# Kernel optimization log

Measured on AMD Instinct MI355X. Metric: run time of the kernel, lower is better.

The kernel has to match this reference:

```python
import jax, jax.numpy as jnp
import numpy as np

SLIDING_WINDOW = 2048
NUM_SINK = 4


def make_mask(q_len, k_len, dtype=jnp.float32):
    # positions of queries in the key axis
    q_pos = jnp.arange(k_len - q_len, k_len)[:, None]  # [Q,1]
    k_pos = jnp.arange(k_len)[None, :]                 # [1,K]
    causal = k_pos <= q_pos
    in_window = k_pos >= (q_pos - SLIDING_WINDOW + 1)
    is_sink = k_pos < NUM_SINK
    allowed = causal & (in_window | is_sink)
    return jnp.where(allowed, jnp.zeros((), dtype), jnp.full((), -jnp.inf, dtype))


def setup_inputs() -> dict:
    key = jax.random.key(0)
    k1, k2, k3 = jax.random.split(key, 3)
    B, H, L, D = 2, 16, 4096, 128
    q = jax.random.normal(k1, (B, H, L, D), dtype=jnp.float32)
    k = jax.random.normal(k2, (B, H, L, D), dtype=jnp.float32)
    v = jax.random.normal(k3, (B, H, L, D), dtype=jnp.float32)
    return {"q": q, "k": k, "v": v}


def reference(q, k, v):
    B, H, L, D = q.shape
    mask = make_mask(L, k.shape[2], q.dtype)  # [L, L] additive
    scale = 1.0 / jnp.sqrt(jnp.asarray(D, q.dtype))
    scores = jnp.einsum('bhqd,bhkd->bhqk', q, k) * scale + mask
    probs = jax.nn.softmax(scores, axis=-1)
    return jnp.einsum('bhqk,bhkd->bhqd', probs, v)
```

## Files before the change

kernel.cpp:

```cpp
#include <hip/hip_runtime.h>

constexpr int Ld = 4096;
constexpr int Dd = 128;
constexpr int BQ = 128;
constexpr int BK = 64;
constexpr int WSZ = 2048;
constexpr int NSINK = 4;
constexpr float QSCALE = 0.08838834764831845f * 1.4426950408889634f;

typedef short bf16x8 __attribute__((ext_vector_type(8)));
typedef float f32x4 __attribute__((ext_vector_type(4)));

#if defined(__has_builtin)
#if __has_builtin(__builtin_amdgcn_exp2f)
#define EXP2(x) __builtin_amdgcn_exp2f(x)
#endif
#endif
#ifndef EXP2
#define EXP2(x) exp2f(x)
#endif

__device__ __forceinline__ unsigned pkbf(float hi, float lo) {
    unsigned r;
    asm("v_cvt_pk_bf16_f32 %0, %1, %2" : "=v"(r) : "v"(lo), "v"(hi));
    return r;
}

__device__ __forceinline__ int rd_off(int row, int d) {
    return row * 128 + ((((d >> 3) ^ row) & 15) << 3) + (d & 7);
}
__device__ __forceinline__ int vt_off(int drow, int key) {
    return drow * 64 + ((((key >> 3) ^ drow) & 7) << 3) + (key & 7);
}
__device__ __forceinline__ int p_off(int row, int key) {
    return row * 64 + ((((key >> 2) ^ ((row & 7) << 1)) & 15) << 2) + (key & 3);
}

typedef const __attribute__((address_space(1))) unsigned int* gas1_t;
typedef __attribute__((address_space(3))) unsigned int* las3_t;
__device__ __forceinline__ void lds16(const void* g, void* l) {
    __builtin_amdgcn_global_load_lds((gas1_t)g, (las3_t)l, 16, 0, 0);
}

__global__ __launch_bounds__(256)
void cvt_kv(const float* __restrict__ Kg, const float* __restrict__ Vg,
            unsigned short* __restrict__ Kw, unsigned short* __restrict__ Vw) {
    __shared__ __align__(16) unsigned short vt[8192];
    const int tid = threadIdx.x;
    const int kb = blockIdx.x * BK;
    const int bh = blockIdx.y;
    const size_t gbase = ((size_t)bh * Ld + kb) * Dd;

    #pragma unroll
    for (int i = 0; i < 8; ++i) {
        int id = tid + i * 256;
        int row = id >> 5;
        int d0 = (id & 31) << 2;
        float4 a = *(const float4*)(Kg + gbase + (size_t)row * Dd + d0);
        *(uint2*)&Kw[gbase + rd_off(row, d0)] =
            make_uint2(pkbf(a.y, a.x), pkbf(a.w, a.z));
    }

    const int vd  = tid & 127;
    const int vkh = tid >> 7;
    const float* vp = Vg + gbase + (size_t)vkh * 32 * Dd + vd;
    float vr[32];
    #pragma unroll
    for (int j = 0; j < 32; ++j) vr[j] = vp[(size_t)j * Dd];
    #pragma unroll
    for (int m2 = 0; m2 < 4; ++m2)
        *(uint4*)&vt[vt_off(vd, vkh * 32 + m2 * 8)] =
            make_uint4(pkbf(vr[m2 * 8 + 1], vr[m2 * 8 + 0]),
                       pkbf(vr[m2 * 8 + 3], vr[m2 * 8 + 2]),
                       pkbf(vr[m2 * 8 + 5], vr[m2 * 8 + 4]),
                       pkbf(vr[m2 * 8 + 7], vr[m2 * 8 + 6]));
    __syncthreads();
    const size_t vbase = ((size_t)bh * (Ld / BK) + blockIdx.x) * (size_t)(BK * Dd);
    #pragma unroll
    for (int i = 0; i < 4; ++i) {
        int j = tid + i * 256;
        *(uint4*)&Vw[vbase + (size_t)j * 8] = *(const uint4*)&vt[j * 8];
    }
}

__global__ __launch_bounds__(256, 2)
void swa_fwd2(const float* __restrict__ Qg, const unsigned short* __restrict__ Kw,
              const unsigned short* __restrict__ Vw, float* __restrict__ Og) {
    __shared__ __align__(16) unsigned short smem[40960];
    unsigned short* Ps  = smem + 32768;
    unsigned short* Qst = smem;

    const int tid  = threadIdx.x;
    const int w    = tid >> 6;
    const int lane = tid & 63;
    const int ml   = lane & 15;
    const int quad = lane >> 4;

    const unsigned wgr = blockIdx.x;
    const unsigned nwg = gridDim.x;
    unsigned wgid = wgr;
    if ((nwg & 7u) == 0u) wgid = (wgr & 7u) * (nwg >> 3) + (wgr >> 3);
    const int tpb   = Ld / BQ;
    const int bh    = (int)(wgid / (unsigned)tpb);
    const int qtile = tpb - 1 - (int)(wgid % (unsigned)tpb);
    const int q0 = qtile * BQ;

    const size_t baseQ = ((size_t)bh * Ld + q0) * Dd;

    #pragma unroll
    for (int i = 0; i < 16; ++i) {
        int idx = tid + i * 256;
        int row = idx >> 5;
        int d0  = (idx & 31) << 2;
        float4 v = *(const float4*)(Qg + baseQ + (size_t)row * Dd + d0);
        *(uint2*)&Qst[rd_off(row, d0)] =
            make_uint2(pkbf(v.y * QSCALE, v.x * QSCALE),
                       pkbf(v.w * QSCALE, v.z * QSCALE));
    }
    __syncthreads();

    bf16x8 qf[2][4];
    #pragma unroll
    for (int g = 0; g < 2; ++g)
        #pragma unroll
        for (int k0 = 0; k0 < 4; ++k0)
            qf[g][k0] = *(const bf16x8*)&Qst[rd_off(w * 32 + g * 16 + ml,
                                                    k0 * 32 + quad * 8)];
    __syncthreads();

    float l_i[2] = {0.f, 0.f};
    f32x4 o_acc[2][8];
    #pragma unroll
    for (int g = 0; g < 2; ++g)
        #pragma unroll
        for (int dt = 0; dt < 8; ++dt)
            o_acc[g][dt] = (f32x4){0.f, 0.f, 0.f, 0.f};

    const int kmin = (q0 - (WSZ - 1)) > 0 ? (q0 - (WSZ - 1)) : 0;
    const int kb_first = (kmin / BK) * BK;
    const bool sink_extra = (kb_first > 0);
    const int nch = (q0 + BQ - kb_first) / BK + (sink_extra ? 1 : 0);

    const int qrow0 = q0 + w * 32 + ml;
    unsigned short* Pw = Ps + w * 2048;

    auto kb_of = [&](int ci) {
        return sink_extra ? (ci == 0 ? 0 : kb_first + (ci - 1) * BK)
                          : kb_first + ci * BK;
    };
    const size_t kwbase = (size_t)bh * Ld * Dd;
    const size_t vwbase = (size_t)bh * (Ld / BK) * (size_t)(BK * Dd);

    auto stage = [&](int ci) {
        const int b = ci & 1;
        const int kb = kb_of(ci);
        const unsigned short* kg = Kw + kwbase + (size_t)kb * Dd + tid * 8;
        unsigned short* kl = smem + b * 8192 + tid * 8;
        const unsigned short* vg = Vw + vwbase + (size_t)(kb >> 6) * (BK * Dd) + tid * 8;
        unsigned short* vl = smem + 16384 + b * 8192 + tid * 8;
        #pragma unroll
        for (int i = 0; i < 4; ++i) lds16(kg + i * 2048, kl + i * 2048);
        #pragma unroll
        for (int i = 0; i < 4; ++i) lds16(vg + i * 2048, vl + i * 2048);
    };

    stage(0);

    for (int ci = 0; ci < nch; ++ci) {
        __syncthreads();
        if (ci + 1 < nch) stage(ci + 1);

        const int kb = kb_of(ci);
        const unsigned short* Ksb = smem + (ci & 1) * 8192;
        const unsigned short* Vtb = smem + 16384 + (ci & 1) * 8192;

        f32x4 s[2][4];
        #pragma unroll
        for (int g = 0; g < 2; ++g)
            #pragma unroll
            for (int t = 0; t < 4; ++t)
                s[g][t] = (f32x4){0.f, 0.f, 0.f, 0.f};
        __builtin_amdgcn_s_setprio(1);
        #pragma unroll
        for (int k0 = 0; k0 < 4; ++k0) {
            bf16x8 ka[4];
            #pragma unroll
            for (int t = 0; t < 4; ++t)
                ka[t] = *(const bf16x8*)&Ksb[rd_off(t * 16 + ml, k0 * 32 + quad * 8)];
            #pragma unroll
            for (int t = 0; t < 4; ++t) {
                s[0][t] = __builtin_amdgcn_mfma_f32_16x16x32_bf16(ka[t], qf[0][k0], s[0][t], 0, 0, 0);
                s[1][t] = __builtin_amdgcn_mfma_f32_16x16x32_bf16(ka[t], qf[1][k0], s[1][t], 0, 0, 0);
            }
        }
        __builtin_amdgcn_s_setprio(0);

        const bool full = (kb + (BK - 1) <= q0) && (kb + (WSZ - BQ) >= q0 - 1);

        #pragma unroll
        for (int g = 0; g < 2; ++g) {
            const int q = qrow0 + g * 16;
            if (!full) {
                #pragma unroll
                for (int t = 0; t < 4; ++t)
                    #pragma unroll
                    for (int r = 0; r < 4; ++r) {
                        int k = kb + t * 16 + quad * 4 + r;
                        bool ok = (k <= q) && ((k + (WSZ - 1) >= q) || (k < NSINK));
                        s[g][t][r] = ok ? s[g][t][r] : -3e38f;
                    }
            }
            float rs = 0.f;
            #pragma unroll
            for (int t = 0; t < 4; ++t)
                #pragma unroll
                for (int r = 0; r < 4; ++r) {
                    float p = EXP2(s[g][t][r]);
                    s[g][t][r] = p;
                    rs += p;
                }
            l_i[g] += rs;

            unsigned short* Pg = Pw + g * 1024;
            #pragma unroll
            for (int t = 0; t < 4; ++t)
                *(uint2*)&Pg[p_off(ml, t * 16 + quad * 4)] =
                    make_uint2(pkbf(s[g][t][1], s[g][t][0]),
                               pkbf(s[g][t][3], s[g][t][2]));
        }

        __builtin_amdgcn_s_setprio(1);
        #pragma unroll
        for (int k0 = 0; k0 < 2; ++k0) {
            bf16x8 pb0 = *(const bf16x8*)&Pw[p_off(ml, k0 * 32 + quad * 8)];
            bf16x8 pb1 = *(const bf16x8*)&Pw[1024 + p_off(ml, k0 * 32 + quad * 8)];
            #pragma unroll
            for (int dt = 0; dt < 8; ++dt) {
                bf16x8 va = *(const bf16x8*)&Vtb[vt_off(dt * 16 + ml, k0 * 32 + quad * 8)];
                o_acc[0][dt] = __builtin_amdgcn_mfma_f32_16x16x32_bf16(va, pb0, o_acc[0][dt], 0, 0, 0);
                o_acc[1][dt] = __builtin_amdgcn_mfma_f32_16x16x32_bf16(va, pb1, o_acc[1][dt], 0, 0, 0);
            }
        }
        __builtin_amdgcn_s_setprio(0);
    }

    #pragma unroll
    for (int g = 0; g < 2; ++g) {
        float lt = l_i[g];
        lt += __shfl_xor(lt, 16);
        lt += __shfl_xor(lt, 32);
        const float inv = 1.f / lt;
        float* op = Og + ((size_t)bh * Ld + (qrow0 + g * 16)) * Dd;
        #pragma unroll
        for (int dt = 0; dt < 8; ++dt) {
            float4 o;
            o.x = o_acc[g][dt][0] * inv;
            o.y = o_acc[g][dt][1] * inv;
            o.z = o_acc[g][dt][2] * inv;
            o.w = o_acc[g][dt][3] * inv;
            *(float4*)(op + dt * 16 + quad * 4) = o;
        }
    }
}

__global__ __launch_bounds__(256, 2)
void swa_fwd(const float* __restrict__ Qg, const float* __restrict__ Kg,
             const float* __restrict__ Vg, float* __restrict__ Og) {
    __shared__ __align__(16) unsigned short smem[24576];
    unsigned short* Ks  = smem;
    unsigned short* Vts = smem + 8192;
    unsigned short* Ps  = smem + 16384;
    unsigned short* Qst = smem;

    const int tid  = threadIdx.x;
    const int w    = tid >> 6;
    const int lane = tid & 63;
    const int ml   = lane & 15;
    const int quad = lane >> 4;

    const int qtile = (int)(gridDim.x - 1u - blockIdx.x);
    const int q0 = qtile * BQ;
    const int bh = blockIdx.y;

    const size_t baseQ  = ((size_t)bh * Ld + q0) * Dd;
    const size_t baseKV = (size_t)bh * Ld * Dd;

    #pragma unroll
    for (int i = 0; i < 16; ++i) {
        int idx = tid + i * 256;
        int row = idx >> 5;
        int d0  = (idx & 31) << 2;
        float4 v = *(const float4*)(Qg + baseQ + (size_t)row * Dd + d0);
        *(uint2*)&Qst[rd_off(row, d0)] =
            make_uint2(pkbf(v.y * QSCALE, v.x * QSCALE),
                       pkbf(v.w * QSCALE, v.z * QSCALE));
    }
    __syncthreads();

    bf16x8 qf[2][4];
    #pragma unroll
    for (int g = 0; g < 2; ++g)
        #pragma unroll
        for (int k0 = 0; k0 < 4; ++k0)
            qf[g][k0] = *(const bf16x8*)&Qst[rd_off(w * 32 + g * 16 + ml,
                                                    k0 * 32 + quad * 8)];

    float l_i[2] = {0.f, 0.f};
    f32x4 o_acc[2][8];
    #pragma unroll
    for (int g = 0; g < 2; ++g)
        #pragma unroll
        for (int dt = 0; dt < 8; ++dt)
            o_acc[g][dt] = (f32x4){0.f, 0.f, 0.f, 0.f};

    const int kmin = (q0 - (WSZ - 1)) > 0 ? (q0 - (WSZ - 1)) : 0;
    const int kb_first = (kmin / BK) * BK;
    const bool sink_extra = (kb_first > 0);
    const int nch = (q0 + BQ - kb_first) / BK + (sink_extra ? 1 : 0);

    const int qrow0 = q0 + w * 32 + ml;
    unsigned short* Pw = Ps + w * 2048;

    float4 kreg[8];
    float  vreg[32];
    const int kr0 = tid >> 5;
    const int kd0 = (tid & 31) << 2;
    const int vd  = tid & 127;
    const int vkh = tid >> 7;

    auto kvload = [&](int kb) {
        const float* kp = Kg + baseKV + (size_t)(kb + kr0) * Dd + kd0;
        #pragma unroll
        for (int i = 0; i < 8; ++i)
            kreg[i] = *(const float4*)(kp + (size_t)i * 8 * Dd);
        const float* vp = Vg + baseKV + (size_t)(kb + vkh * 32) * Dd + vd;
        #pragma unroll
        for (int j = 0; j < 32; ++j)
            vreg[j] = vp[(size_t)j * Dd];
    };
    auto kb_of = [&](int ci) {
        return sink_extra ? (ci == 0 ? 0 : kb_first + (ci - 1) * BK)
                          : kb_first + ci * BK;
    };

    kvload(kb_of(0));

    for (int ci = 0; ci < nch; ++ci) {
        const int kb = kb_of(ci);
        __syncthreads();
        #pragma unroll
        for (int i = 0; i < 8; ++i)
            *(uint2*)&Ks[rd_off(kr0 + i * 8, kd0)] =
                make_uint2(pkbf(kreg[i].y, kreg[i].x),
                           pkbf(kreg[i].w, kreg[i].z));
        #pragma unroll
        for (int m2 = 0; m2 < 4; ++m2) {
            *(uint4*)&Vts[vt_off(vd, vkh * 32 + m2 * 8)] =
                make_uint4(pkbf(vreg[m2 * 8 + 1], vreg[m2 * 8 + 0]),
                           pkbf(vreg[m2 * 8 + 3], vreg[m2 * 8 + 2]),
                           pkbf(vreg[m2 * 8 + 5], vreg[m2 * 8 + 4]),
                           pkbf(vreg[m2 * 8 + 7], vreg[m2 * 8 + 6]));
        }
        __syncthreads();
        if (ci + 1 < nch) kvload(kb_of(ci + 1));

        f32x4 s[2][4];
        #pragma unroll
        for (int g = 0; g < 2; ++g)
            #pragma unroll
            for (int t = 0; t < 4; ++t)
                s[g][t] = (f32x4){0.f, 0.f, 0.f, 0.f};
        #pragma unroll
        for (int k0 = 0; k0 < 4; ++k0) {
            bf16x8 ka[4];
            #pragma unroll
            for (int t = 0; t < 4; ++t)
                ka[t] = *(const bf16x8*)&Ks[rd_off(t * 16 + ml, k0 * 32 + quad * 8)];
            #pragma unroll
            for (int t = 0; t < 4; ++t) {
                s[0][t] = __builtin_amdgcn_mfma_f32_16x16x32_bf16(ka[t], qf[0][k0], s[0][t], 0, 0, 0);
                s[1][t] = __builtin_amdgcn_mfma_f32_16x16x32_bf16(ka[t], qf[1][k0], s[1][t], 0, 0, 0);
            }
        }

        const bool full = (kb + (BK - 1) <= q0) && (kb + (WSZ - BQ) >= q0 - 1);

        #pragma unroll
        for (int g = 0; g < 2; ++g) {
            const int q = qrow0 + g * 16;
            if (!full) {
                #pragma unroll
                for (int t = 0; t < 4; ++t)
                    #pragma unroll
                    for (int r = 0; r < 4; ++r) {
                        int k = kb + t * 16 + quad * 4 + r;
                        bool ok = (k <= q) && ((k + (WSZ - 1) >= q) || (k < NSINK));
                        s[g][t][r] = ok ? s[g][t][r] : -3e38f;
                    }
            }
            float rs = 0.f;
            #pragma unroll
            for (int t = 0; t < 4; ++t)
                #pragma unroll
                for (int r = 0; r < 4; ++r) {
                    float p = EXP2(s[g][t][r]);
                    s[g][t][r] = p;
                    rs += p;
                }
            l_i[g] += rs;

            unsigned short* Pg = Pw + g * 1024;
            #pragma unroll
            for (int t = 0; t < 4; ++t)
                *(uint2*)&Pg[p_off(ml, t * 16 + quad * 4)] =
                    make_uint2(pkbf(s[g][t][1], s[g][t][0]),
                               pkbf(s[g][t][3], s[g][t][2]));
        }

        #pragma unroll
        for (int k0 = 0; k0 < 2; ++k0) {
            bf16x8 pb0 = *(const bf16x8*)&Pw[p_off(ml, k0 * 32 + quad * 8)];
            bf16x8 pb1 = *(const bf16x8*)&Pw[1024 + p_off(ml, k0 * 32 + quad * 8)];
            #pragma unroll
            for (int dt = 0; dt < 8; ++dt) {
                bf16x8 va = *(const bf16x8*)&Vts[vt_off(dt * 16 + ml, k0 * 32 + quad * 8)];
                o_acc[0][dt] = __builtin_amdgcn_mfma_f32_16x16x32_bf16(va, pb0, o_acc[0][dt], 0, 0, 0);
                o_acc[1][dt] = __builtin_amdgcn_mfma_f32_16x16x32_bf16(va, pb1, o_acc[1][dt], 0, 0, 0);
            }
        }
    }

    #pragma unroll
    for (int g = 0; g < 2; ++g) {
        float lt = l_i[g];
        lt += __shfl_xor(lt, 16);
        lt += __shfl_xor(lt, 32);
        const float inv = 1.f / lt;
        float* op = Og + ((size_t)bh * Ld + (qrow0 + g * 16)) * Dd;
        #pragma unroll
        for (int dt = 0; dt < 8; ++dt) {
            float4 o;
            o.x = o_acc[g][dt][0] * inv;
            o.y = o_acc[g][dt][1] * inv;
            o.z = o_acc[g][dt][2] * inv;
            o.w = o_acc[g][dt][3] * inv;
            *(float4*)(op + dt * 16 + quad * 4) = o;
        }
    }
}

extern "C" void kernel_launch(void* const* d_in, const int* in_sizes, int n_in,
                              void* d_out, int out_size, void* d_ws, size_t ws_size,
                              hipStream_t stream) {
    const float* q = (const float*)d_in[0];
    const float* k = (const float*)d_in[1];
    const float* v = (const float*)d_in[2];
    float* o = (float*)d_out;
    const int bhn = in_sizes[0] / (Ld * Dd);
    const size_t elems = (size_t)bhn * Ld * Dd;
    const size_t need = 2 * elems * sizeof(unsigned short);
    if (d_ws != nullptr && ws_size >= need) {
        unsigned short* Kw = (unsigned short*)d_ws;
        unsigned short* Vw = Kw + elems;
        cvt_kv<<<dim3(Ld / BK, bhn), dim3(256, 1, 1), 0, stream>>>(k, v, Kw, Vw);
        swa_fwd2<<<dim3((unsigned)(bhn * (Ld / BQ))), dim3(256, 1, 1), 0, stream>>>(q, Kw, Vw, o);
    } else {
        dim3 grid(Ld / BQ, bhn);
        swa_fwd<<<grid, dim3(256, 1, 1), 0, stream>>>(q, k, v, o);
    }
}
```

Measured before the change: 340.0 us.

## Halve key tile to 32, raise occupancy to four workgroups, remap XCD scheduling

Shrinks the key/value chunk from 64 to 32 rows, which halves shared memory use so the launch bound can ask for four workgroups per CU instead of two. The pre-converted V layout, P staging swizzles and per-chunk MFMA loops are rewritten for 32-key tiles. The workgroup-to-(head, q-tile) mapping is hardcoded for a 1024-block grid to spread causal work evenly across XCDs. The fallback kernel keeps 64-wide chunks with local layout helpers. Smaller chunks mean twice as many barriers and softmax passes per key and less work per chunk to hide load latency.

```diff
diff --git a/kernel.cpp b/kernel.cpp
--- a/kernel.cpp
+++ b/kernel.cpp
@@ -3,7 +3,7 @@
 constexpr int Ld = 4096;
 constexpr int Dd = 128;
 constexpr int BQ = 128;
-constexpr int BK = 64;
+constexpr int BK = 32;
 constexpr int WSZ = 2048;
 constexpr int NSINK = 4;
 constexpr float QSCALE = 0.08838834764831845f * 1.4426950408889634f;
@@ -29,11 +29,11 @@
 __device__ __forceinline__ int rd_off(int row, int d) {
     return row * 128 + ((((d >> 3) ^ row) & 15) << 3) + (d & 7);
 }
-__device__ __forceinline__ int vt_off(int drow, int key) {
-    return drow * 64 + ((((key >> 3) ^ drow) & 7) << 3) + (key & 7);
-}
-__device__ __forceinline__ int p_off(int row, int key) {
-    return row * 64 + ((((key >> 2) ^ ((row & 7) << 1)) & 15) << 2) + (key & 3);
+__device__ __forceinline__ int vt32(int drow, int key) {
+    return drow * 32 + ((((key >> 3) ^ drow) & 3) << 3) + (key & 7);
+}
+__device__ __forceinline__ int p32(int row, int key) {
+    return row * 32 + ((((key >> 3) ^ (row >> 1)) & 3) << 3) + (key & 7);
 }
 
 typedef const __attribute__((address_space(1))) unsigned int* gas1_t;
@@ -45,14 +45,14 @@
 __global__ __launch_bounds__(256)
 void cvt_kv(const float* __restrict__ Kg, const float* __restrict__ Vg,
             unsigned short* __restrict__ Kw, unsigned short* __restrict__ Vw) {
-    __shared__ __align__(16) unsigned short vt[8192];
+    __shared__ __align__(16) unsigned short vt[4096];
     const int tid = threadIdx.x;
     const int kb = blockIdx.x * BK;
     const int bh = blockIdx.y;
     const size_t gbase = ((size_t)bh * Ld + kb) * Dd;
 
     #pragma unroll
-    for (int i = 0; i < 8; ++i) {
+    for (int i = 0; i < 4; ++i) {
         int id = tid + i * 256;
         int row = id >> 5;
         int d0 = (id & 31) << 2;
@@ -63,13 +63,13 @@
 
     const int vd  = tid & 127;
     const int vkh = tid >> 7;
-    const float* vp = Vg + gbase + (size_t)vkh * 32 * Dd + vd;
-    float vr[32];
-    #pragma unroll
-    for (int j = 0; j < 32; ++j) vr[j] = vp[(size_t)j * Dd];
-    #pragma unroll
-    for (int m2 = 0; m2 < 4; ++m2)
-        *(uint4*)&vt[vt_off(vd, vkh * 32 + m2 * 8)] =
+    const float* vp = Vg + gbase + (size_t)vkh * 16 * Dd + vd;
+    float vr[16];
+    #pragma unroll
+    for (int j = 0; j < 16; ++j) vr[j] = vp[(size_t)j * Dd];
+    #pragma unroll
+    for (int m2 = 0; m2 < 2; ++m2)
+        *(uint4*)&vt[vt32(vd, vkh * 16 + m2 * 8)] =
             make_uint4(pkbf(vr[m2 * 8 + 1], vr[m2 * 8 + 0]),
                        pkbf(vr[m2 * 8 + 3], vr[m2 * 8 + 2]),
                        pkbf(vr[m2 * 8 + 5], vr[m2 * 8 + 4]),
@@ -77,17 +77,17 @@
     __syncthreads();
     const size_t vbase = ((size_t)bh * (Ld / BK) + blockIdx.x) * (size_t)(BK * Dd);
     #pragma unroll
-    for (int i = 0; i < 4; ++i) {
+    for (int i = 0; i < 2; ++i) {
         int j = tid + i * 256;
         *(uint4*)&Vw[vbase + (size_t)j * 8] = *(const uint4*)&vt[j * 8];
     }
 }
 
-__global__ __launch_bounds__(256, 2)
+__global__ __launch_bounds__(256, 4)
 void swa_fwd2(const float* __restrict__ Qg, const unsigned short* __restrict__ Kw,
               const unsigned short* __restrict__ Vw, float* __restrict__ Og) {
-    __shared__ __align__(16) unsigned short smem[40960];
-    unsigned short* Ps  = smem + 32768;
+    __shared__ __align__(16) unsigned short smem[20480];
+    unsigned short* Ps  = smem + 16384;
     unsigned short* Qst = smem;
 
     const int tid  = threadIdx.x;
@@ -97,12 +97,23 @@
     const int quad = lane >> 4;
 
     const unsigned wgr = blockIdx.x;
-    const unsigned nwg = gridDim.x;
-    unsigned wgid = wgr;
-    if ((nwg & 7u) == 0u) wgid = (wgr & 7u) * (nwg >> 3) + (wgr >> 3);
-    const int tpb   = Ld / BQ;
-    const int bh    = (int)(wgid / (unsigned)tpb);
-    const int qtile = tpb - 1 - (int)(wgid % (unsigned)tpb);
+    int bh, qtile;
+    if (gridDim.x == 1024u) {
+        const unsigned xcd = wgr & 7u;
+        const unsigned idx = wgr >> 3;
+        const unsigned rr  = idx >> 5;
+        const unsigned p   = idx & 31u;
+        unsigned rank = (rr == 0u) ? p
+                      : (rr == 1u) ? ((15u - p) & 31u)
+                      : (rr == 2u) ? ((16u + p) & 31u)
+                                   : ((31u - p) & 31u);
+        bh    = (int)(xcd * 4u + rr);
+        qtile = 31 - (int)rank;
+    } else {
+        const int tpb = Ld / BQ;
+        bh    = (int)(wgr / (unsigned)tpb);
+        qtile = tpb - 1 - (int)(wgr % (unsigned)tpb);
+    }
     const int q0 = qtile * BQ;
 
     const size_t baseQ = ((size_t)bh * Ld + q0) * Dd;
@@ -142,7 +153,7 @@
     const int nch = (q0 + BQ - kb_first) / BK + (sink_extra ? 1 : 0);
 
     const int qrow0 = q0 + w * 32 + ml;
-    unsigned short* Pw = Ps + w * 2048;
+    unsigned short* Pw = Ps + w * 1024;
 
     auto kb_of = [&](int ci) {
         return sink_extra ? (ci == 0 ? 0 : kb_first + (ci - 1) * BK)
@@ -155,13 +166,13 @@
         const int b = ci & 1;
         const int kb = kb_of(ci);
         const unsigned short* kg = Kw + kwbase + (size_t)kb * Dd + tid * 8;
-        unsigned short* kl = smem + b * 8192 + tid * 8;
-        const unsigned short* vg = Vw + vwbase + (size_t)(kb >> 6) * (BK * Dd) + tid * 8;
-        unsigned short* vl = smem + 16384 + b * 8192 + tid * 8;
-        #pragma unroll
-        for (int i = 0; i < 4; ++i) lds16(kg + i * 2048, kl + i * 2048);
-        #pragma unroll
-        for (int i = 0; i < 4; ++i) lds16(vg + i * 2048, vl + i * 2048);
+        unsigned short* kl = smem + b * 4096 + tid * 8;
+        const unsigned short* vg = Vw + vwbase + (size_t)(kb >> 5) * (BK * Dd) + tid * 8;
+        unsigned short* vl = smem + 8192 + b * 4096 + tid * 8;
+        lds16(kg, kl);
+        lds16(kg + 2048, kl + 2048);
+        lds16(vg, vl);
+        lds16(vg + 2048, vl + 2048);
     };
 
     stage(0);
@@ -171,38 +182,35 @@
         if (ci + 1 < nch) stage(ci + 1);
 
         const int kb = kb_of(ci);
-        const unsigned short* Ksb = smem + (ci & 1) * 8192;
-        const unsigned short* Vtb = smem + 16384 + (ci & 1) * 8192;
-
-        f32x4 s[2][4];
+        const unsigned short* Ksb = smem + (ci & 1) * 4096;
+        const unsigned short* Vtb = smem + 8192 + (ci & 1) * 4096;
+
+        f32x4 s[2][2];
         #pragma unroll
         for (int g = 0; g < 2; ++g)
             #pragma unroll
-            for (int t = 0; t < 4; ++t)
+            for (int t = 0; t < 2; ++t)
                 s[g][t] = (f32x4){0.f, 0.f, 0.f, 0.f};
         __builtin_amdgcn_s_setprio(1);
         #pragma unroll
         for (int k0 = 0; k0 < 4; ++k0) {
-            bf16x8 ka[4];
-            #pragma unroll
-            for (int t = 0; t < 4; ++t)
-                ka[t] = *(const bf16x8*)&Ksb[rd_off(t * 16 + ml, k0 * 32 + quad * 8)];
-            #pragma unroll
-            for (int t = 0; t < 4; ++t) {
-                s[0][t] = __builtin_amdgcn_mfma_f32_16x16x32_bf16(ka[t], qf[0][k0], s[0][t], 0, 0, 0);
-                s[1][t] = __builtin_amdgcn_mfma_f32_16x16x32_bf16(ka[t], qf[1][k0], s[1][t], 0, 0, 0);
-            }
+            bf16x8 ka0 = *(const bf16x8*)&Ksb[rd_off(ml,      k0 * 32 + quad * 8)];
+            bf16x8 ka1 = *(const bf16x8*)&Ksb[rd_off(16 + ml, k0 * 32 + quad * 8)];
+            s[0][0] = __builtin_amdgcn_mfma_f32_16x16x32_bf16(ka0, qf[0][k0], s[0][0], 0, 0, 0);
+            s[1][0] = __builtin_amdgcn_mfma_f32_16x16x32_bf16(ka0, qf[1][k0], s[1][0], 0, 0, 0);
+            s[0][1] = __builtin_amdgcn_mfma_f32_16x16x32_bf16(ka1, qf[0][k0], s[0][1], 0, 0, 0);
+            s[1][1] = __builtin_amdgcn_mfma_f32_16x16x32_bf16(ka1, qf[1][k0], s[1][1], 0, 0, 0);
         }
         __builtin_amdgcn_s_setprio(0);
 
-        const bool full = (kb + (BK - 1) <= q0) && (kb + (WSZ - BQ) >= q0 - 1);
+        const bool full = (kb + (BK - 1) <= q0) && (kb >= q0 + BQ - WSZ);
 
         #pragma unroll
         for (int g = 0; g < 2; ++g) {
             const int q = qrow0 + g * 16;
             if (!full) {
                 #pragma unroll
-                for (int t = 0; t < 4; ++t)
+                for (int t = 0; t < 2; ++t)
                     #pragma unroll
                     for (int r = 0; r < 4; ++r) {
                         int k = kb + t * 16 + quad * 4 + r;
@@ -212,7 +220,7 @@
             }
             float rs = 0.f;
             #pragma unroll
-            for (int t = 0; t < 4; ++t)
+            for (int t = 0; t < 2; ++t)
                 #pragma unroll
                 for (int r = 0; r < 4; ++r) {
                     float p = EXP2(s[g][t][r]);
@@ -221,22 +229,21 @@
                 }
             l_i[g] += rs;
 
-            unsigned short* Pg = Pw + g * 1024;
-            #pragma unroll
-            for (int t = 0; t < 4; ++t)
-                *(uint2*)&Pg[p_off(ml, t * 16 + quad * 4)] =
+            unsigned short* Pg = Pw + g * 512;
+            #pragma unroll
+            for (int t = 0; t < 2; ++t)
+                *(uint2*)&Pg[p32(ml, t * 16 + quad * 4)] =
                     make_uint2(pkbf(s[g][t][1], s[g][t][0]),
                                pkbf(s[g][t][3], s[g][t][2]));
         }
 
         __builtin_amdgcn_s_setprio(1);
-        #pragma unroll
-        for (int k0 = 0; k0 < 2; ++k0) {
-            bf16x8 pb0 = *(const bf16x8*)&Pw[p_off(ml, k0 * 32 + quad * 8)];
-            bf16x8 pb1 = *(const bf16x8*)&Pw[1024 + p_off(ml, k0 * 32 + quad * 8)];
+        {
+            bf16x8 pb0 = *(const bf16x8*)&Pw[p32(ml, quad * 8)];
+            bf16x8 pb1 = *(const bf16x8*)&Pw[512 + p32(ml, quad * 8)];
             #pragma unroll
             for (int dt = 0; dt < 8; ++dt) {
-                bf16x8 va = *(const bf16x8*)&Vtb[vt_off(dt * 16 + ml, k0 * 32 + quad * 8)];
+                bf16x8 va = *(const bf16x8*)&Vtb[vt32(dt * 16 + ml, quad * 8)];
                 o_acc[0][dt] = __builtin_amdgcn_mfma_f32_16x16x32_bf16(va, pb0, o_acc[0][dt], 0, 0, 0);
                 o_acc[1][dt] = __builtin_amdgcn_mfma_f32_16x16x32_bf16(va, pb1, o_acc[1][dt], 0, 0, 0);
             }
@@ -279,11 +286,18 @@
     const int quad = lane >> 4;
 
     const int qtile = (int)(gridDim.x - 1u - blockIdx.x);
-    const int q0 = qtile * BQ;
+    const int q0 = qtile * BQ * 1;
     const int bh = blockIdx.y;
 
     const size_t baseQ  = ((size_t)bh * Ld + q0) * Dd;
     const size_t baseKV = (size_t)bh * Ld * Dd;
+
+    auto vt_off = [](int drow, int key) {
+        return drow * 64 + ((((key >> 3) ^ drow) & 7) << 3) + (key & 7);
+    };
+    auto p_off = [](int row, int key) {
+        return row * 64 + ((((key >> 2) ^ ((row & 7) << 1)) & 15) << 2) + (key & 3);
+    };
 
     #pragma unroll
     for (int i = 0; i < 16; ++i) {
@@ -314,9 +328,9 @@
             o_acc[g][dt] = (f32x4){0.f, 0.f, 0.f, 0.f};
 
     const int kmin = (q0 - (WSZ - 1)) > 0 ? (q0 - (WSZ - 1)) : 0;
-    const int kb_first = (kmin / BK) * BK;
+    const int kb_first = (kmin / 64) * 64;
     const bool sink_extra = (kb_first > 0);
-    const int nch = (q0 + BQ - kb_first) / BK + (sink_extra ? 1 : 0);
+    const int nch = (q0 + BQ - kb_first) / 64 + (sink_extra ? 1 : 0);
 
     const int qrow0 = q0 + w * 32 + ml;
     unsigned short* Pw = Ps + w * 2048;
@@ -339,8 +353,8 @@
             vreg[j] = vp[(size_t)j * Dd];
     };
     auto kb_of = [&](int ci) {
-        return sink_extra ? (ci == 0 ? 0 : kb_first + (ci - 1) * BK)
-                          : kb_first + ci * BK;
+        return sink_extra ? (ci == 0 ? 0 : kb_first + (ci - 1) * 64)
+                          : kb_first + ci * 64;
     };
 
     kvload(kb_of(0));
@@ -383,7 +397,7 @@
             }
         }
 
-        const bool full = (kb + (BK - 1) <= q0) && (kb + (WSZ - BQ) >= q0 - 1);
+        const bool full = (kb + 63 <= q0) && (kb >= q0 + BQ - WSZ);
 
         #pragma unroll
         for (int g = 0; g < 2; ++g) {
```

Result: slower. 418.5 us (+23.1%).

## Use 256-row query tiles with 8 waves and XCD-aware balanced tile mapping

Applied to the files above, without the earlier changes.

Doubles the query tile to 256 rows and runs the main kernel with 512 threads (8 waves), so each K/V chunk staged into LDS is shared by twice as many queries. It adds a hardcoded grid remapping for 512 workgroups that places four heads on each XCD and pairs long and short tiles to balance work. The P buffer per wave is halved, and P·V now runs one 16-row group at a time, which reuses the smaller buffer in exchange for more LDS round trips. The full-block mask test is rewritten for the larger tile. Risks include lower occupancy from the larger block and more per-query work spent on partially masked chunks at the window edges.

```diff
diff --git a/kernel.cpp b/kernel.cpp
--- a/kernel.cpp
+++ b/kernel.cpp
@@ -2,7 +2,7 @@
 
 constexpr int Ld = 4096;
 constexpr int Dd = 128;
-constexpr int BQ = 128;
+constexpr int BQ = 256;
 constexpr int BK = 64;
 constexpr int WSZ = 2048;
 constexpr int NSINK = 4;
@@ -83,7 +83,7 @@
     }
 }
 
-__global__ __launch_bounds__(256, 2)
+__global__ __launch_bounds__(512, 4)
 void swa_fwd2(const float* __restrict__ Qg, const unsigned short* __restrict__ Kw,
               const unsigned short* __restrict__ Vw, float* __restrict__ Og) {
     __shared__ __align__(16) unsigned short smem[40960];
@@ -97,19 +97,28 @@
     const int quad = lane >> 4;
 
     const unsigned wgr = blockIdx.x;
-    const unsigned nwg = gridDim.x;
-    unsigned wgid = wgr;
-    if ((nwg & 7u) == 0u) wgid = (wgr & 7u) * (nwg >> 3) + (wgr >> 3);
-    const int tpb   = Ld / BQ;
-    const int bh    = (int)(wgid / (unsigned)tpb);
-    const int qtile = tpb - 1 - (int)(wgid % (unsigned)tpb);
+    int bh, qtile;
+    if (gridDim.x == 512u) {
+        const unsigned xcd = wgr & 7u;
+        const unsigned idx = wgr >> 3;
+        const unsigned rr  = idx >> 5;
+        const unsigned p   = idx & 31u;
+        const unsigned j   = (rr == 0u) ? p : (63u - p);
+        const unsigned rank = j >> 2;
+        bh    = (int)(xcd * 4u + (j & 3u));
+        qtile = 15 - (int)rank;
+    } else {
+        const int tpb = Ld / BQ;
+        bh    = (int)(wgr / (unsigned)tpb);
+        qtile = tpb - 1 - (int)(wgr % (unsigned)tpb);
+    }
     const int q0 = qtile * BQ;
 
     const size_t baseQ = ((size_t)bh * Ld + q0) * Dd;
 
     #pragma unroll
     for (int i = 0; i < 16; ++i) {
-        int idx = tid + i * 256;
+        int idx = tid + i * 512;
         int row = idx >> 5;
         int d0  = (idx & 31) << 2;
         float4 v = *(const float4*)(Qg + baseQ + (size_t)row * Dd + d0);
@@ -142,7 +151,7 @@
     const int nch = (q0 + BQ - kb_first) / BK + (sink_extra ? 1 : 0);
 
     const int qrow0 = q0 + w * 32 + ml;
-    unsigned short* Pw = Ps + w * 2048;
+    unsigned short* Pw = Ps + w * 1024;
 
     auto kb_of = [&](int ci) {
         return sink_extra ? (ci == 0 ? 0 : kb_first + (ci - 1) * BK)
@@ -158,10 +167,10 @@
         unsigned short* kl = smem + b * 8192 + tid * 8;
         const unsigned short* vg = Vw + vwbase + (size_t)(kb >> 6) * (BK * Dd) + tid * 8;
         unsigned short* vl = smem + 16384 + b * 8192 + tid * 8;
-        #pragma unroll
-        for (int i = 0; i < 4; ++i) lds16(kg + i * 2048, kl + i * 2048);
-        #pragma unroll
-        for (int i = 0; i < 4; ++i) lds16(vg + i * 2048, vl + i * 2048);
+        lds16(kg, kl);
+        lds16(kg + 4096, kl + 4096);
+        lds16(vg, vl);
+        lds16(vg + 4096, vl + 4096);
     };
 
     stage(0);
@@ -195,7 +204,7 @@
         }
         __builtin_amdgcn_s_setprio(0);
 
-        const bool full = (kb + (BK - 1) <= q0) && (kb + (WSZ - BQ) >= q0 - 1);
+        const bool full = (kb + (BK - 1) <= q0) && (kb >= q0 + BQ - WSZ);
 
         #pragma unroll
         for (int g = 0; g < 2; ++g) {
@@ -220,28 +229,27 @@
                     rs += p;
                 }
             l_i[g] += rs;
-
-            unsigned short* Pg = Pw + g * 1024;
-            #pragma unroll
-            for (int t = 0; t < 4; ++t)
-                *(uint2*)&Pg[p_off(ml, t * 16 + quad * 4)] =
+        }
+
+        #pragma unroll
+        for (int g = 0; g < 2; ++g) {
+            #pragma unroll
+            for (int t = 0; t < 4; ++t)
+                *(uint2*)&Pw[p_off(ml, t * 16 + quad * 4)] =
                     make_uint2(pkbf(s[g][t][1], s[g][t][0]),
                                pkbf(s[g][t][3], s[g][t][2]));
-        }
-
-        __builtin_amdgcn_s_setprio(1);
-        #pragma unroll
-        for (int k0 = 0; k0 < 2; ++k0) {
-            bf16x8 pb0 = *(const bf16x8*)&Pw[p_off(ml, k0 * 32 + quad * 8)];
-            bf16x8 pb1 = *(const bf16x8*)&Pw[1024 + p_off(ml, k0 * 32 + quad * 8)];
-            #pragma unroll
-            for (int dt = 0; dt < 8; ++dt) {
-                bf16x8 va = *(const bf16x8*)&Vtb[vt_off(dt * 16 + ml, k0 * 32 + quad * 8)];
-                o_acc[0][dt] = __builtin_amdgcn_mfma_f32_16x16x32_bf16(va, pb0, o_acc[0][dt], 0, 0, 0);
-                o_acc[1][dt] = __builtin_amdgcn_mfma_f32_16x16x32_bf16(va, pb1, o_acc[1][dt], 0, 0, 0);
-            }
-        }
-        __builtin_amdgcn_s_setprio(0);
+            __builtin_amdgcn_s_setprio(1);
+            #pragma unroll
+            for (int k0 = 0; k0 < 2; ++k0) {
+                bf16x8 pb = *(const bf16x8*)&Pw[p_off(ml, k0 * 32 + quad * 8)];
+                #pragma unroll
+                for (int dt = 0; dt < 8; ++dt) {
+                    bf16x8 va = *(const bf16x8*)&Vtb[vt_off(dt * 16 + ml, k0 * 32 + quad * 8)];
+                    o_acc[g][dt] = __builtin_amdgcn_mfma_f32_16x16x32_bf16(va, pb, o_acc[g][dt], 0, 0, 0);
+                }
+            }
+            __builtin_amdgcn_s_setprio(0);
+        }
     }
 
     #pragma unroll
@@ -266,6 +274,7 @@
 __global__ __launch_bounds__(256, 2)
 void swa_fwd(const float* __restrict__ Qg, const float* __restrict__ Kg,
              const float* __restrict__ Vg, float* __restrict__ Og) {
+    constexpr int BQF = 128;
     __shared__ __align__(16) unsigned short smem[24576];
     unsigned short* Ks  = smem;
     unsigned short* Vts = smem + 8192;
@@ -279,7 +288,7 @@
     const int quad = lane >> 4;
 
     const int qtile = (int)(gridDim.x - 1u - blockIdx.x);
-    const int q0 = qtile * BQ;
+    const int q0 = qtile * BQF;
     const int bh = blockIdx.y;
 
     const size_t baseQ  = ((size_t)bh * Ld + q0) * Dd;
@@ -314,9 +323,9 @@
             o_acc[g][dt] = (f32x4){0.f, 0.f, 0.f, 0.f};
 
     const int kmin = (q0 - (WSZ - 1)) > 0 ? (q0 - (WSZ - 1)) : 0;
-    const int kb_first = (kmin / BK) * BK;
+    const int kb_first = (kmin / 64) * 64;
     const bool sink_extra = (kb_first > 0);
-    const int nch = (q0 + BQ - kb_first) / BK + (sink_extra ? 1 : 0);
+    const int nch = (q0 + BQF - kb_first) / 64 + (sink_extra ? 1 : 0);
 
     const int qrow0 = q0 + w * 32 + ml;
     unsigned short* Pw = Ps + w * 2048;
@@ -339,8 +348,8 @@
             vreg[j] = vp[(size_t)j * Dd];
     };
     auto kb_of = [&](int ci) {
-        return sink_extra ? (ci == 0 ? 0 : kb_first + (ci - 1) * BK)
-                          : kb_first + ci * BK;
+        return sink_extra ? (ci == 0 ? 0 : kb_first + (ci - 1) * 64)
+                          : kb_first + ci * 64;
     };
 
     kvload(kb_of(0));
@@ -383,7 +392,7 @@
             }
         }
 
-        const bool full = (kb + (BK - 1) <= q0) && (kb + (WSZ - BQ) >= q0 - 1);
+        const bool full = (kb + 63 <= q0) && (kb >= q0 + BQF - WSZ);
 
         #pragma unroll
         for (int g = 0; g < 2; ++g) {
@@ -463,9 +472,9 @@
         unsigned short* Kw = (unsigned short*)d_ws;
         unsigned short* Vw = Kw + elems;
         cvt_kv<<<dim3(Ld / BK, bhn), dim3(256, 1, 1), 0, stream>>>(k, v, Kw, Vw);
-        swa_fwd2<<<dim3((unsigned)(bhn * (Ld / BQ))), dim3(256, 1, 1), 0, stream>>>(q, Kw, Vw, o);
+        swa_fwd2<<<dim3((unsigned)(bhn * (Ld / BQ))), dim3(512, 1, 1), 0, stream>>>(q, Kw, Vw, o);
     } else {
-        dim3 grid(Ld / BQ, bhn);
+        dim3 grid(Ld / 128, bhn);
         swa_fwd<<<grid, dim3(256, 1, 1), 0, stream>>>(q, k, v, o);
     }
 }
```

Result: slower. 478.3 us (+40.7%).

## Load V fragments directly from global into registers, shrink LDS for 3 WGs/CU

Applied to the files above, without the earlier changes.

The V preprocessing kernel now writes V in the MFMA fragment order. The main kernel can then load each lane's V operand straight from global memory into registers instead of staging it through LDS. This halves the shared-memory footprint, which allows raising launch bounds from 2 to 3 workgroups per CU for more occupancy. The full-tile mask condition is also tightened, which may send some boundary tiles through the masking path. The trade-off is higher register pressure and global-load latency exposed inside the loop, since V is no longer double-buffered.

```diff
diff --git a/kernel.cpp b/kernel.cpp
--- a/kernel.cpp
+++ b/kernel.cpp
@@ -79,15 +79,16 @@
     #pragma unroll
     for (int i = 0; i < 4; ++i) {
         int j = tid + i * 256;
-        *(uint4*)&Vw[vbase + (size_t)j * 8] = *(const uint4*)&vt[j * 8];
-    }
-}
-
-__global__ __launch_bounds__(256, 2)
+        *(uint4*)&Vw[vbase + (size_t)j * 8] =
+            *(const uint4*)&vt[vt_off(j >> 3, (j & 7) * 8)];
+    }
+}
+
+__global__ __launch_bounds__(256, 3)
 void swa_fwd2(const float* __restrict__ Qg, const unsigned short* __restrict__ Kw,
               const unsigned short* __restrict__ Vw, float* __restrict__ Og) {
-    __shared__ __align__(16) unsigned short smem[40960];
-    unsigned short* Ps  = smem + 32768;
+    __shared__ __align__(16) unsigned short smem[24576];
+    unsigned short* Ps  = smem + 16384;
     unsigned short* Qst = smem;
 
     const int tid  = threadIdx.x;
@@ -149,19 +150,15 @@
                           : kb_first + ci * BK;
     };
     const size_t kwbase = (size_t)bh * Ld * Dd;
-    const size_t vwbase = (size_t)bh * (Ld / BK) * (size_t)(BK * Dd);
+    const unsigned short* vwb = Vw + (size_t)bh * Ld * Dd + ml * 64 + quad * 8;
 
     auto stage = [&](int ci) {
         const int b = ci & 1;
         const int kb = kb_of(ci);
         const unsigned short* kg = Kw + kwbase + (size_t)kb * Dd + tid * 8;
-        unsigned short* kl = smem + b * 8192 + tid * 8;
-        const unsigned short* vg = Vw + vwbase + (size_t)(kb >> 6) * (BK * Dd) + tid * 8;
-        unsigned short* vl = smem + 16384 + b * 8192 + tid * 8;
+        unsigned short* kl = smem + b * 4096 * 2 + tid * 8;
         #pragma unroll
         for (int i = 0; i < 4; ++i) lds16(kg + i * 2048, kl + i * 2048);
-        #pragma unroll
-        for (int i = 0; i < 4; ++i) lds16(vg + i * 2048, vl + i * 2048);
     };
 
     stage(0);
@@ -172,7 +169,12 @@
 
         const int kb = kb_of(ci);
         const unsigned short* Ksb = smem + (ci & 1) * 8192;
-        const unsigned short* Vtb = smem + 16384 + (ci & 1) * 8192;
+        const unsigned short* vtile = vwb + (size_t)(kb >> 6) * (BK * Dd);
+
+        uint4 v0[8];
+        #pragma unroll
+        for (int dt = 0; dt < 8; ++dt)
+            v0[dt] = *(const uint4*)(vtile + dt * 1024);
 
         f32x4 s[2][4];
         #pragma unroll
@@ -195,7 +197,7 @@
         }
         __builtin_amdgcn_s_setprio(0);
 
-        const bool full = (kb + (BK - 1) <= q0) && (kb + (WSZ - BQ) >= q0 - 1);
+        const bool full = (kb + (BK - 1) <= q0) && (kb >= q0 + BQ - WSZ);
 
         #pragma unroll
         for (int g = 0; g < 2; ++g) {
@@ -229,14 +231,26 @@
                                pkbf(s[g][t][3], s[g][t][2]));
         }
 
+        uint4 v1[8];
+        #pragma unroll
+        for (int dt = 0; dt < 8; ++dt)
+            v1[dt] = *(const uint4*)(vtile + dt * 1024 + 32);
+
         __builtin_amdgcn_s_setprio(1);
-        #pragma unroll
-        for (int k0 = 0; k0 < 2; ++k0) {
-            bf16x8 pb0 = *(const bf16x8*)&Pw[p_off(ml, k0 * 32 + quad * 8)];
-            bf16x8 pb1 = *(const bf16x8*)&Pw[1024 + p_off(ml, k0 * 32 + quad * 8)];
+        {
+            bf16x8 pb0 = *(const bf16x8*)&Pw[p_off(ml, quad * 8)];
+            bf16x8 pb1 = *(const bf16x8*)&Pw[1024 + p_off(ml, quad * 8)];
             #pragma unroll
             for (int dt = 0; dt < 8; ++dt) {
-                bf16x8 va = *(const bf16x8*)&Vtb[vt_off(dt * 16 + ml, k0 * 32 + quad * 8)];
+                bf16x8 va = __builtin_bit_cast(bf16x8, v0[dt]);
+                o_acc[0][dt] = __builtin_amdgcn_mfma_f32_16x16x32_bf16(va, pb0, o_acc[0][dt], 0, 0, 0);
+                o_acc[1][dt] = __builtin_amdgcn_mfma_f32_16x16x32_bf16(va, pb1, o_acc[1][dt], 0, 0, 0);
+            }
+            pb0 = *(const bf16x8*)&Pw[p_off(ml, 32 + quad * 8)];
+            pb1 = *(const bf16x8*)&Pw[1024 + p_off(ml, 32 + quad * 8)];
+            #pragma unroll
+            for (int dt = 0; dt < 8; ++dt) {
+                bf16x8 va = __builtin_bit_cast(bf16x8, v1[dt]);
                 o_acc[0][dt] = __builtin_amdgcn_mfma_f32_16x16x32_bf16(va, pb0, o_acc[0][dt], 0, 0, 0);
                 o_acc[1][dt] = __builtin_amdgcn_mfma_f32_16x16x32_bf16(va, pb1, o_acc[1][dt], 0, 0, 0);
             }
@@ -383,7 +397,7 @@
             }
         }
 
-        const bool full = (kb + (BK - 1) <= q0) && (kb + (WSZ - BQ) >= q0 - 1);
+        const bool full = (kb + (BK - 1) <= q0) && (kb >= q0 + BQ - WSZ);
 
         #pragma unroll
         for (int g = 0; g < 2; ++g) {
```

After: 669.6 us. 97.0% more time.
